# Optimization experiments

Hardware: AMD Instinct MI355X
Metric: run time of the kernel (lower is better)

## Reference

```python
import math
import jax, jax.numpy as jnp
import numpy as np

GRAIN = 300   # bilinear / grain dim (gpconv output channels)
PAD = 4       # explicit zero padding before each conv1d / conv2d
POOL = 40     # adaptive pool target (mf_model_pool_dim)

def conv1d_k2(x, w, b):
    # x: [B, L, Cin], w: [Cout, Cin, 2] -> [B, L-1, Cout]
    return (jnp.einsum('blc,oc->blo', x[:, :-1], w[:, :, 0])
            + jnp.einsum('blc,oc->blo', x[:, 1:], w[:, :, 1]) + b)

def kmax_last(x, k):
    # torch-style k-max pooling: top-k values along last axis, original order kept
    idx = jnp.sort(jax.lax.top_k(x, k)[1], axis=-1)
    return jnp.take_along_axis(x, idx, axis=-1)

def kmax_len(x, k):
    # k-max pooling over the length axis (axis=1) of [B, L, C]
    return jnp.swapaxes(kmax_last(jnp.swapaxes(x, 1, 2), k), 1, 2)

def adaptive_max_1d(x, out, axis):
    # torch AdaptiveMaxPool semantics along one axis; windows precomputed statically
    L = x.shape[axis]
    r = np.arange(out)
    starts = (r * L) // out
    ends = -((-(r + 1) * L) // out)
    maxw = int((ends - starts).max())
    off = starts[:, None] + np.arange(maxw)[None, :]
    mask = jnp.asarray(off < ends[:, None])
    idxs = np.minimum(off, L - 1)
    xm = jnp.moveaxis(x, axis, -1)
    g = jnp.where(mask, xm[..., idxs], -jnp.inf)
    return jnp.moveaxis(g.max(-1), -1, axis)

def conv2d_p4(x, w, b):
    y = jax.lax.conv_general_dilated(x, w, (1, 1), [(PAD, PAD), (PAD, PAD)],
                                     dimension_numbers=('NCHW', 'OIHW', 'NCHW'))
    return y + b[None, :, None, None]

def gp_tower(x, w1, b1, w2, b2, w3, b3, k1, k2):
    # multigranular conv tower: zero-pad(4) -> conv1d(k=2) -> tanh -> k-max pool
    g0 = kmax_last(x, GRAIN)                      # [B, L, 300]
    def block(z, w, b, k):
        z = jnp.pad(z, ((0, 0), (PAD, PAD), (0, 0)))
        return kmax_len(jnp.tanh(conv1d_k2(z, w, b)), k)
    p1 = block(x, w1, b1, k1)                     # [B, k1, 300]
    p2 = block(p1, w2, b2, k2)                    # [B, k2, 300]
    p3 = block(p2, w3, b3, 1)                     # [B, 1, 300]
    return jnp.concatenate([g0, p1, p2, p3], axis=1)

def _forward(query, pos_doc, neg_docs, qw1, qb1, qw2, qb2, qw3, qb3,
             dw1, db1, dw2, db2, dw3, db3, bw, bb,
             mw1, mb1, mw2, mb2, mw3, mb3, lw, lb):
    B, Lq, _ = query.shape
    S, _, Ld, _ = neg_docs.shape
    kq1, kq2 = max(4, math.ceil(2 * Lq / 3)), max(4, math.ceil(Lq / 3))
    kd1, kd2 = max(4, math.ceil(2 * Ld / 3)), max(4, math.ceil(Ld / 3))
    qg = gp_tower(query, qw1, qb1, qw2, qb2, qw3, qb3, kq1, kq2)   # [B, Nq, 300]
    docs = jnp.concatenate([pos_doc[None], neg_docs], 0).reshape((S + 1) * B, Ld, -1)
    dg = gp_tower(docs, dw1, db1, dw2, db2, dw3, db3, kd1, kd2)    # [(S+1)B, Nd, 300]
    Nq, Nd = qg.shape[1], dg.shape[1]
    dg = dg.reshape(S + 1, B, Nd, GRAIN)
    # batched bilinear matching + sigmoid (replaces the O(Nq*Nd) per-pair loop)
    qt = jnp.einsum('bqd,de->bqe', qg, bw)
    M = jax.nn.sigmoid(jnp.einsum('bqe,sbje->sbqj', qt, dg) + bb[0])
    M = M.reshape((S + 1) * B, Nq, Nd)
    x = adaptive_max_1d(adaptive_max_1d(M, POOL, 1), POOL, 2)[:, None]  # [N,1,40,40]
    for w, b in ((mw1, mb1), (mw2, mb2), (mw3, mb3)):
        x = jax.nn.sigmoid(conv2d_p4(x, w, b))
        x = adaptive_max_1d(adaptive_max_1d(x, POOL, 2), POOL, 3)
        x = x.max(axis=1, keepdims=True)          # k-max(k=1) over channels
    feat = x[:, 0]                                # [N, 40, 40]
    h = jax.nn.sigmoid(jnp.einsum('nij,j->ni', feat, lw[0]) + lb[0])
    s = jax.nn.sigmoid(h @ lw[0] + lb[0])
    return s.reshape(S + 1, B)                    # row 0 = pos-doc scores

def setup_inputs():
    ks = jax.random.split(jax.random.key(0), 26)
    def n(i, shape, s=0.05):
        return jax.random.normal(ks[i], shape, dtype=jnp.float32) * s
    return dict(
        query=jax.random.normal(ks[0], (16, 239, 1024), dtype=jnp.float32),
        pos_doc=jax.random.normal(ks[1], (16, 479, 1024), dtype=jnp.float32),
        neg_docs=jax.random.normal(ks[2], (4, 16, 479, 1024), dtype=jnp.float32),
        qw1=n(3, (300, 1024, 2)), qb1=n(4, (300,)),
        qw2=n(5, (300, 300, 2)), qb2=n(6, (300,)),
        qw3=n(7, (300, 300, 2)), qb3=n(8, (300,)),
        dw1=n(9, (300, 1024, 2)), db1=n(10, (300,)),
        dw2=n(11, (300, 300, 2)), db2=n(12, (300,)),
        dw3=n(13, (300, 300, 2)), db3=n(14, (300,)),
        bw=n(15, (300, 300)), bb=n(16, (1,)),
        mw1=n(17, (50, 1, 2, 2)), mb1=n(18, (50,)),
        mw2=n(19, (50, 1, 2, 2)), mb2=n(20, (50,)),
        mw3=n(21, (50, 1, 2, 2)), mb3=n(22, (50,)),
        lw=n(23, (1, 40)), lb=n(24, (1,)),
    )

def reference(query, pos_doc, neg_docs, qw1, qb1, qw2, qb2, qw3, qb3,
              dw1, db1, dw2, db2, dw3, db3, bw, bb,
              mw1, mb1, mw2, mb2, mw3, mb3, lw, lb):
    return _forward(query, pos_doc, neg_docs, qw1, qb1, qw2, qb2, qw3, qb3,
                    dw1, db1, dw2, db2, dw3, db3, bw, bb,
                    mw1, mb1, mw2, mb2, mw3, mb3, lw, lb)
```

## Files before the change

### kernel.cpp

```cpp
#include <hip/hip_runtime.h>
#include <hip/hip_bf16.h>
#include <math.h>

typedef unsigned long long ull;
typedef unsigned int uint;
typedef unsigned short ushort_t;

typedef short bf16x8 __attribute__((ext_vector_type(8)));
typedef float floatx4 __attribute__((ext_vector_type(4)));

__device__ inline ushort_t f2b(float f) {
    uint u = __float_as_uint(f);
    u = u + 0x7fffu + ((u >> 16) & 1u);
    return (ushort_t)(u >> 16);
}

__device__ inline uint kmap16(ushort_t u) {
    return (u & 0x8000u) ? (uint)((~u) & 0xFFFFu) : (uint)(u | 0x8000u);
}
__device__ inline ushort_t kinv16(uint k) {
    return (k & 0x8000u) ? (ushort_t)(k ^ 0x8000u) : (ushort_t)((~k) & 0xFFFFu);
}

__device__ inline void async_copy16(const void* g, void* l) {
    __builtin_amdgcn_global_load_lds(
        (const __attribute__((address_space(1))) void*)g,
        (__attribute__((address_space(3))) void*)l, 16, 0, 0);
}

__global__ void prep_w2_kernel(const float* __restrict__ w, ushort_t* __restrict__ Wb,
                               int C, int CPAD) {
    int total = 320 * 2 * CPAD;
    for (int i = blockIdx.x * blockDim.x + threadIdx.x; i < total;
         i += gridDim.x * blockDim.x) {
        int n = i / (2 * CPAD);
        int rem = i - n * 2 * CPAD;
        int t = rem / CPAD, c = rem - t * CPAD;
        float v = (n < 300 && c < C) ? w[((size_t)n * C + c) * 2 + t] : 0.f;
        Wb[i] = f2b(v);
    }
}

__global__ void prep_bw_kernel(const float* __restrict__ bw, ushort_t* __restrict__ bwb) {
    int i = blockIdx.x * 256 + threadIdx.x;
    if (i >= 320 * 320) return;
    int e = i / 320, d = i - e * 320;
    bwb[i] = (e < 300 && d < 300) ? f2b(bw[d * 300 + e]) : (ushort_t)0;
}

__global__ __launch_bounds__(256) void x_pad_bf16_kernel(
    const float* __restrict__ src, const float* __restrict__ src2, int split_n,
    long long s_nstr, int Lin, ushort_t* __restrict__ dst, int rows)
{
    int r = blockIdx.x, n = blockIdx.y;
    const float* sp = (split_n > 0 && n >= split_n)
                          ? src2 + (size_t)(n - split_n) * s_nstr
                          : src + (size_t)n * s_nstr;
    int g = r - 4;
    ushort_t* dp = dst + ((size_t)n * rows + r) * 1024;
    int c = threadIdx.x * 4;
    ushort4 o = {0, 0, 0, 0};
    if (g >= 0 && g < Lin) {
        float4 v = *(const float4*)&sp[(size_t)g * 1024 + c];
        o.x = f2b(v.x); o.y = f2b(v.y); o.z = f2b(v.z); o.w = f2b(v.w);
    }
    *(ushort4*)&dp[c] = o;
}

template <int CP>
__global__ __launch_bounds__(256, 2) void conv_lds_kernel(
    const ushort_t* __restrict__ xq, long long xq_nstr,
    const ushort_t* __restrict__ xd, long long xd_nstr,
    const ushort_t* __restrict__ Wq, const ushort_t* __restrict__ Wd,
    const float* __restrict__ bq, const float* __restrict__ bd,
    int Lout_q, int Lout_d, int mtiles_q,
    ushort_t* __restrict__ yt)
{
    constexpr int CH = CP / 32;
    constexpr int K2 = 2 * CP;
    __shared__ ushort_t Abuf[2][65 * 32];

    int mt = blockIdx.x, n = blockIdx.y;
    bool isq = (n < 16);
    if (isq && mt >= mtiles_q) return;
    const ushort_t* x = isq ? xq + (size_t)n * xq_nstr
                            : xd + (size_t)(n - 16) * xd_nstr;
    const ushort_t* W = isq ? Wq : Wd;
    const float* bias = isq ? bq : bd;
    int Lout = isq ? Lout_q : Lout_d;
    int l0 = mt * 64;

    int tid = threadIdx.x, wid = tid >> 6, lane = tid & 63;
    int wn = wid * 80;
    int lrow = lane & 15, quad = lane >> 4;

    const ushort_t* g0 = x + (size_t)(l0 + (tid >> 2)) * CP + (tid & 3) * 8;
    const ushort_t* g1 = x + (size_t)(l0 + 64) * CP + (tid & 3) * 8;

    const ushort_t* Bb = W + (size_t)(wn + lrow) * K2 + quad * 8;

    floatx4 acc[4][5];
#pragma unroll
    for (int i = 0; i < 4; i++)
#pragma unroll
        for (int j = 0; j < 5; j++) acc[i][j] = (floatx4){0.f, 0.f, 0.f, 0.f};

    {
        char* lb = (char*)&Abuf[0][0];
        async_copy16(g0, lb + wid * 1024);
        if (tid < 4) async_copy16(g1, lb + 4096);
    }

    for (int c = 0; c < CH; c++) {
        __syncthreads();
        int c0 = c * 32;

        bf16x8 bfr[2][5];
#pragma unroll
        for (int t = 0; t < 2; t++)
#pragma unroll
            for (int ns = 0; ns < 5; ns++)
                bfr[t][ns] = *(const bf16x8*)&Bb[(size_t)(ns * 16) * K2 + t * CP + c0];

        if (c + 1 < CH) {
            char* lb = (char*)&Abuf[(c + 1) & 1][0];
            async_copy16(g0 + c0 + 32, lb + wid * 1024);
            if (tid < 4) async_copy16(g1 + c0 + 32, lb + 4096);
        }

        const char* ab = (const char*)&Abuf[c & 1][0];
        bf16x8 af[2][4];
#pragma unroll
        for (int t = 0; t < 2; t++)
#pragma unroll
            for (int ms = 0; ms < 4; ms++)
                af[t][ms] = *(const bf16x8*)(ab + (ms * 16 + lrow + t) * 64 + quad * 16);

#pragma unroll
        for (int t = 0; t < 2; t++)
#pragma unroll
            for (int ms = 0; ms < 4; ms++)
#pragma unroll
                for (int ns = 0; ns < 5; ns++)
                    acc[ms][ns] = __builtin_amdgcn_mfma_f32_16x16x32_bf16(
                        af[t][ms], bfr[t][ns], acc[ms][ns], 0, 0, 0);
    }

    ushort_t* yp = yt + (size_t)n * 488 * 320;
#pragma unroll
    for (int ns = 0; ns < 5; ns++) {
        int o = wn + ns * 16 + lrow;
        if (o >= 300) continue;
        float bo = bias[o];
#pragma unroll
        for (int ms = 0; ms < 4; ms++)
#pragma unroll
            for (int r = 0; r < 4; r++) {
                int l = l0 + ms * 16 + quad * 4 + r;
                if (l < Lout)
                    yp[(size_t)l * 320 + o] = f2b(tanhf(acc[ms][ns][r] + bo));
            }
    }
}

template <int EPT>
__global__ __launch_bounds__(256) void topk16_kernel(
    const ushort_t* __restrict__ src, int CC,
    long long s_n, long long s_c, long long s_e,
    int L, int k,
    ushort_t* __restrict__ out1, long long o1_off, long long o1_n,
    long long o1_c, long long o1_e,
    ushort_t* __restrict__ out2, long long o2_off, long long o2_n,
    long long o2_c, long long o2_e)
{
    __shared__ uint sbuf[257];
    __shared__ uint wtot[4];
    __shared__ uint bsel[2];
    __shared__ uint wsum[4];

    int row = blockIdx.x;
    int n = row / CC, c = row - n * CC;
    const ushort_t* sp = src + (size_t)n * s_n + (size_t)c * s_c;

    int tid = threadIdx.x, lane = tid & 63, wid = tid >> 6;
    int base = tid * EPT;

    uint key[EPT];
    if (EPT == 4 && s_e == 1) {
        ushort4 v = *(const ushort4*)&sp[base];
        key[0] = kmap16(v.x); key[1] = kmap16(v.y);
        key[2] = kmap16(v.z); key[3] = kmap16(v.w);
    } else {
#pragma unroll
        for (int e = 0; e < EPT; e++) {
            int i = base + e;
            key[e] = (i < L) ? kmap16(sp[(size_t)i * s_e]) : 0u;
        }
    }

    uint pmask = 0, pval = 0, rem = (uint)k;
#pragma unroll
    for (int shift = 8; shift >= 0; shift -= 8) {
        sbuf[tid] = 0;
        __syncthreads();
#pragma unroll
        for (int e = 0; e < EPT; e++) {
            int i = base + e;
            if (i < L && (key[e] & pmask) == pval)
                atomicAdd(&sbuf[(key[e] >> shift) & 255], 1u);
        }
        __syncthreads();
        uint sfx = sbuf[tid];
#pragma unroll
        for (int off = 1; off < 64; off <<= 1) {
            uint u2 = __shfl_down(sfx, off);
            if (lane + off < 64) sfx += u2;
        }
        if (lane == 0) wtot[wid] = sfx;
        __syncthreads();
        uint hi = 0;
        for (int w = wid + 1; w < 4; w++) hi += wtot[w];
        sbuf[tid] = sfx + hi;
        if (tid == 0) sbuf[256] = 0;
        __syncthreads();
        uint cg = sbuf[tid], cgn = sbuf[tid + 1];
        if (cg >= rem && cgn < rem) { bsel[0] = (uint)tid; bsel[1] = rem - cgn; }
        __syncthreads();
        pval |= bsel[0] << shift;
        pmask |= 0xFFu << shift;
        rem = bsel[1];
        __syncthreads();
    }

    const uint T = pval;
    uint gtc = 0, eqc = 0;
#pragma unroll
    for (int e = 0; e < EPT; e++) {
        int i = base + e;
        if (i < L) {
            gtc += (key[e] > T) ? 1u : 0u;
            eqc += (key[e] == T) ? 1u : 0u;
        }
    }
    uint pack = (gtc << 16) | eqc;
    uint incl = pack;
#pragma unroll
    for (int off = 1; off < 64; off <<= 1) {
        uint u2 = __shfl_up(incl, off);
        if (lane >= off) incl += u2;
    }
    uint excl = incl - pack;
    if (lane == 63) wsum[wid] = incl;
    __syncthreads();
    uint badd = 0;
    for (int w = 0; w < wid; w++) badd += wsum[w];
    excl += badd;
    uint gt_before = excl >> 16, eq_before = excl & 0xffffu;

    ushort_t* dp1 = out1 + (size_t)o1_off + (size_t)n * o1_n + (size_t)c * o1_c;
    ushort_t* dp2 = out2 ? out2 + (size_t)o2_off + (size_t)n * o2_n + (size_t)c * o2_c
                         : (ushort_t*)0;
#pragma unroll
    for (int e = 0; e < EPT; e++) {
        int i = base + e;
        if (i >= L) break;
        uint kk = key[e];
        if (kk > T) {
            uint pos = gt_before + (eq_before < rem ? eq_before : rem);
            ushort_t v = kinv16(kk);
            dp1[(size_t)pos * o1_e] = v;
            if (dp2) dp2[(size_t)pos * o2_e] = v;
            gt_before++;
        } else if (kk == T) {
            if (eq_before < rem) {
                uint pos = gt_before + eq_before;
                ushort_t v = kinv16(kk);
                dp1[(size_t)pos * o1_e] = v;
                if (dp2) dp2[(size_t)pos * o2_e] = v;
            }
            eq_before++;
        }
    }
}

__global__ __launch_bounds__(256) void qt_mfma_kernel(
    const ushort_t* __restrict__ qgb, const ushort_t* __restrict__ bwb,
    ushort_t* __restrict__ qtb)
{
    int mt = blockIdx.x, b = blockIdx.y;
    int tid = threadIdx.x, wid = tid >> 6, lane = tid & 63;
    int wn = wid * 80, lrow = lane & 15, quad = lane >> 4;

    const ushort_t* A = qgb + ((size_t)b * 480 + mt * 48 + lrow) * 320 + quad * 8;
    const ushort_t* B = bwb + (size_t)(wn + lrow) * 320 + quad * 8;

    floatx4 acc[3][5];
#pragma unroll
    for (int i = 0; i < 3; i++)
#pragma unroll
        for (int j = 0; j < 5; j++) acc[i][j] = (floatx4){0.f, 0.f, 0.f, 0.f};

#pragma unroll 5
    for (int c0 = 0; c0 < 320; c0 += 32) {
        bf16x8 af[3], bfr[5];
#pragma unroll
        for (int ms = 0; ms < 3; ms++)
            af[ms] = *(const bf16x8*)&A[(size_t)(ms * 16) * 320 + c0];
#pragma unroll
        for (int ns = 0; ns < 5; ns++)
            bfr[ns] = *(const bf16x8*)&B[(size_t)(ns * 16) * 320 + c0];
#pragma unroll
        for (int ms = 0; ms < 3; ms++)
#pragma unroll
            for (int ns = 0; ns < 5; ns++)
                acc[ms][ns] = __builtin_amdgcn_mfma_f32_16x16x32_bf16(
                    af[ms], bfr[ns], acc[ms][ns], 0, 0, 0);
    }

    ushort_t* out = qtb + ((size_t)b * 480 + mt * 48) * 320;
#pragma unroll
    for (int ms = 0; ms < 3; ms++)
#pragma unroll
        for (int ns = 0; ns < 5; ns++)
#pragma unroll
            for (int r = 0; r < 4; r++)
                out[(size_t)(ms * 16 + quad * 4 + r) * 320 + wn + ns * 16 + lrow] =
                    f2b(acc[ms][ns][r]);
}

__global__ __launch_bounds__(256) void mpool_mfma_kernel(
    const ushort_t* __restrict__ qtb16, const ushort_t* __restrict__ dgb16,
    const float* __restrict__ bb, float* __restrict__ mp)
{
    __shared__ float pool[2 * 12 * 192];

    int jb = blockIdx.x;
    int qb = blockIdx.y;
    int n  = blockIdx.z;
    int b  = n & 15;

    int tid = threadIdx.x;
    int wid = tid >> 6, lane = tid & 63;
    int wm2 = wid >> 1;
    int wm = wm2 * 48, wn = (wid & 1) * 96;
    int lrow = lane & 15, quad = lane >> 4;

    const ushort_t* Abase = qtb16 + ((size_t)b * 480 + qb * 96 + wm) * 320 + quad * 8;
    const ushort_t* Bbase = dgb16 + ((size_t)n * 960 + jb * 192 + wn) * 320 + quad * 8;

    floatx4 acc[3][6];
#pragma unroll
    for (int i = 0; i < 3; i++)
#pragma unroll
        for (int j = 0; j < 6; j++) acc[i][j] = (floatx4){0.f, 0.f, 0.f, 0.f};

#pragma unroll 2
    for (int c0 = 0; c0 < 320; c0 += 32) {
        bf16x8 af[3], bfr[6];
#pragma unroll
        for (int mt = 0; mt < 3; mt++)
            af[mt] = *(const bf16x8*)&Abase[(size_t)(mt * 16 + lrow) * 320 + c0];
#pragma unroll
        for (int nt = 0; nt < 6; nt++)
            bfr[nt] = *(const bf16x8*)&Bbase[(size_t)(nt * 16 + lrow) * 320 + c0];
#pragma unroll
        for (int mt = 0; mt < 3; mt++)
#pragma unroll
            for (int nt = 0; nt < 6; nt++)
                acc[mt][nt] = __builtin_amdgcn_mfma_f32_16x16x32_bf16(
                    af[mt], bfr[nt], acc[mt][nt], 0, 0, 0);
    }

#pragma unroll
    for (int mt = 0; mt < 3; mt++) {
        int g = mt * 4 + quad;
#pragma unroll
        for (int nt = 0; nt < 6; nt++) {
            floatx4 a = acc[mt][nt];
            float rm = fmaxf(fmaxf(a[0], a[1]), fmaxf(a[2], a[3]));
            pool[(wm2 * 12 + g) * 192 + wn + nt * 16 + lrow] = rm;
        }
    }
    __syncthreads();

    if (tid < 64) {
        int qw = tid >> 3, jw = tid & 7;
        int slab = qw >> 2, w = qw & 3;
        float m = -INFINITY;
        const float* pp = &pool[(slab * 12 + w * 3) * 192 + jw * 24];
        for (int g = 0; g < 3; g++)
            for (int cc = 0; cc < 24; cc++)
                m = fmaxf(m, pp[g * 192 + cc]);
        float sig = 1.f / (1.f + expf(-(m + bb[0])));
        mp[(size_t)n * 1600 + (size_t)(qb * 8 + qw) * 40 + (jb * 8 + jw)] = sig;
    }
}

#define OCG 10
__global__ __launch_bounds__(256) void convblock_atomic_kernel(
    const float* __restrict__ X, const float* __restrict__ w,
    const float* __restrict__ bias, uint* __restrict__ Y)
{
    __shared__ float xp[48 * 48];
    __shared__ float ys[47 * 47];
    __shared__ float t1[40 * 47];
    __shared__ float outacc[1600];

    int n = blockIdx.x, t = threadIdx.x;
    int oc0 = blockIdx.y * OCG;
    const float* xn = X + (size_t)n * 1600;
    for (int i = t; i < 48 * 48; i += 256) {
        int r = i / 48, c = i - r * 48;
        int rr = r - 4, cc = c - 4;
        xp[i] = (rr >= 0 && rr < 40 && cc >= 0 && cc < 40) ? xn[rr * 40 + cc] : 0.f;
    }
    for (int i = t; i < 1600; i += 256) outacc[i] = 0.f;
    __syncthreads();

    for (int oc = oc0; oc < oc0 + OCG; oc++) {
        float w00 = w[oc * 4 + 0], w01 = w[oc * 4 + 1];
        float w10 = w[oc * 4 + 2], w11 = w[oc * 4 + 3];
        float bo = bias[oc];
        for (int i = t; i < 47 * 47; i += 256) {
            int r = i / 47, c = i - r * 47;
            float v = xp[r * 48 + c] * w00 + xp[r * 48 + c + 1] * w01
                    + xp[(r + 1) * 48 + c] * w10 + xp[(r + 1) * 48 + c + 1] * w11 + bo;
            ys[i] = 1.f / (1.f + expf(-v));
        }
        __syncthreads();
        for (int i = t; i < 40 * 47; i += 256) {
            int r = i / 47, c = i - r * 47;
            int s = (47 * r) / 40, e = (47 * (r + 1) + 39) / 40;
            float m = ys[s * 47 + c];
            for (int x = s + 1; x < e; x++) m = fmaxf(m, ys[x * 47 + c]);
            t1[i] = m;
        }
        __syncthreads();
        for (int i = t; i < 1600; i += 256) {
            int r = i / 40, c = i - r * 40;
            int s = (47 * c) / 40, e = (47 * (c + 1) + 39) / 40;
            float m = t1[r * 47 + s];
            for (int x = s + 1; x < e; x++) m = fmaxf(m, t1[r * 47 + x]);
            outacc[i] = fmaxf(outacc[i], m);
        }
        __syncthreads();
    }
    for (int i = t; i < 1600; i += 256)
        atomicMax(&Y[(size_t)n * 1600 + i], __float_as_uint(outacc[i]));
}

__global__ __launch_bounds__(64) void head_kernel(
    const float* __restrict__ feat, const float* __restrict__ lw,
    const float* __restrict__ lb, float* __restrict__ out)
{
    __shared__ float hs[40];
    int n = blockIdx.x, t = threadIdx.x;
    const float* f = feat + (size_t)n * 1600;
    if (t < 40) {
        float a = 0.f;
        for (int j = 0; j < 40; j++) a += f[t * 40 + j] * lw[j];
        hs[t] = 1.f / (1.f + expf(-(a + lb[0])));
    }
    __syncthreads();
    if (t == 0) {
        float a = 0.f;
        for (int i = 0; i < 40; i++) a += hs[i] * lw[i];
        out[n] = 1.f / (1.f + expf(-(a + lb[0])));
    }
}

extern "C" void kernel_launch(void* const* d_in, const int* in_sizes, int n_in,
                              void* d_out, int out_size, void* d_ws, size_t ws_size,
                              hipStream_t stream) {
    const float* query    = (const float*)d_in[0];
    const float* pos_doc  = (const float*)d_in[1];
    const float* neg_docs = (const float*)d_in[2];
    const float* qw1 = (const float*)d_in[3];  const float* qb1 = (const float*)d_in[4];
    const float* qw2 = (const float*)d_in[5];  const float* qb2 = (const float*)d_in[6];
    const float* qw3 = (const float*)d_in[7];  const float* qb3 = (const float*)d_in[8];
    const float* dw1 = (const float*)d_in[9];  const float* db1 = (const float*)d_in[10];
    const float* dw2 = (const float*)d_in[11]; const float* db2 = (const float*)d_in[12];
    const float* dw3 = (const float*)d_in[13]; const float* db3 = (const float*)d_in[14];
    const float* bw  = (const float*)d_in[15]; const float* bb  = (const float*)d_in[16];
    const float* mw1 = (const float*)d_in[17]; const float* mb1 = (const float*)d_in[18];
    const float* mw2 = (const float*)d_in[19]; const float* mb2 = (const float*)d_in[20];
    const float* mw3 = (const float*)d_in[21]; const float* mb3 = (const float*)d_in[22];
    const float* lw  = (const float*)d_in[23]; const float* lb  = (const float*)d_in[24];

    float* ws = (float*)d_ws;
    ushort_t* qw1b  = (ushort_t*)(ws + 0);
    ushort_t* qw2b  = (ushort_t*)(ws + 327680);
    ushort_t* qw3b  = (ushort_t*)(ws + 430080);
    ushort_t* dw1b  = (ushort_t*)(ws + 532480);
    ushort_t* dw2b  = (ushort_t*)(ws + 860160);
    ushort_t* dw3b  = (ushort_t*)(ws + 962560);
    ushort_t* bwb   = (ushort_t*)(ws + 1064960);
    ushort_t* qgb16 = (ushort_t*)(ws + 1116160);
    ushort_t* dgb16 = (ushort_t*)(ws + 2344960);
    ushort_t* yt    = (ushort_t*)(ws + 14632960);
    ushort_t* qxb   = (ushort_t*)(ws + 22128640);
    ushort_t* p1q   = (ushort_t*)(ws + 22128640);
    ushort_t* p2q   = (ushort_t*)(ws + 22640640);
    ushort_t* dxb   = (ushort_t*)(ws + 24291328);
    ushort_t* p1d   = (ushort_t*)(ws + 24291328);
    ushort_t* p2d   = (ushort_t*)(ws + 28899328);
    ushort_t* qtb16 = (ushort_t*)(ws + 31459328);
    float*    mp    = ws + 32688128;
    float*    ya    = ws + 32816128;
    float*    yb    = ws + 32944128;
    float*    yc    = ws + 33072128;

    prep_w2_kernel<<<1280, 256, 0, stream>>>(qw1, qw1b, 1024, 1024);
    prep_w2_kernel<<<400, 256, 0, stream>>>(qw2, qw2b, 300, 320);
    prep_w2_kernel<<<400, 256, 0, stream>>>(qw3, qw3b, 300, 320);
    prep_w2_kernel<<<1280, 256, 0, stream>>>(dw1, dw1b, 1024, 1024);
    prep_w2_kernel<<<400, 256, 0, stream>>>(dw2, dw2b, 300, 320);
    prep_w2_kernel<<<400, 256, 0, stream>>>(dw3, dw3b, 300, 320);
    prep_bw_kernel<<<400, 256, 0, stream>>>(bw, bwb);

    {
        dim3 g(264, 16);
        x_pad_bf16_kernel<<<g, 256, 0, stream>>>(query, nullptr, 0,
                                                 239LL * 1024, 239, qxb, 264);
    }
    {
        dim3 g(520, 80);
        x_pad_bf16_kernel<<<g, 256, 0, stream>>>(pos_doc, neg_docs, 16,
                                                 479LL * 1024, 479, dxb, 520);
    }

    topk16_kernel<4><<<16 * 239, 256, 0, stream>>>(
        qxb + 4 * 1024, 239, 264LL * 1024, 1024, 1, 1024, 300,
        qgb16, 0, 480LL * 320, 320, 1,
        nullptr, 0, 0, 0, 0);
    topk16_kernel<4><<<80 * 479, 256, 0, stream>>>(
        dxb + 4 * 1024, 479, 520LL * 1024, 1024, 1, 1024, 300,
        dgb16, 0, 960LL * 320, 320, 1,
        nullptr, 0, 0, 0, 0);

    {
        dim3 g(8, 96);
        conv_lds_kernel<1024><<<g, 256, 0, stream>>>(
            qxb, 264LL * 1024, dxb, 520LL * 1024,
            qw1b, dw1b, qb1, db1, 246, 486, 4, yt);
    }

    hipMemsetAsync(p1q, 0, 16 * 200 * 320 * 2, stream);
    hipMemsetAsync(p2q, 0, 16 * 104 * 320 * 2, stream);
    hipMemsetAsync(p1d, 0, (size_t)80 * 360 * 320 * 2, stream);
    hipMemsetAsync(p2d, 0, (size_t)80 * 200 * 320 * 2, stream);
    hipMemsetAsync(ya, 0, 80 * 1600 * 4, stream);
    hipMemsetAsync(yb, 0, 80 * 1600 * 4, stream);
    hipMemsetAsync(yc, 0, 80 * 1600 * 4, stream);

    topk16_kernel<1><<<16 * 300, 256, 0, stream>>>(
        yt, 300, 488LL * 320, 1, 320, 246, 160,
        qgb16, 239LL * 320, 480LL * 320, 1, 320,
        p1q, 4LL * 320, 200LL * 320, 1, 320);
    topk16_kernel<2><<<80 * 300, 256, 0, stream>>>(
        yt + (size_t)16 * 488 * 320, 300, 488LL * 320, 1, 320, 486, 320,
        dgb16, 479LL * 320, 960LL * 320, 1, 320,
        p1d, 4LL * 320, 360LL * 320, 1, 320);

    {
        dim3 g(6, 96);
        conv_lds_kernel<320><<<g, 256, 0, stream>>>(
            p1q, 200LL * 320, p1d, 360LL * 320,
            qw2b, dw2b, qb2, db2, 167, 327, 3, yt);
    }

    topk16_kernel<1><<<16 * 300, 256, 0, stream>>>(
        yt, 300, 488LL * 320, 1, 320, 167, 80,
        qgb16, 399LL * 320, 480LL * 320, 1, 320,
        p2q, 4LL * 320, 104LL * 320, 1, 320);
    topk16_kernel<2><<<80 * 300, 256, 0, stream>>>(
        yt + (size_t)16 * 488 * 320, 300, 488LL * 320, 1, 320, 327, 160,
        dgb16, 799LL * 320, 960LL * 320, 1, 320,
        p2d, 4LL * 320, 200LL * 320, 1, 320);

    {
        dim3 g(3, 96);
        conv_lds_kernel<320><<<g, 256, 0, stream>>>(
            p2q, 104LL * 320, p2d, 200LL * 320,
            qw3b, dw3b, qb3, db3, 87, 167, 2, yt);
    }

    topk16_kernel<1><<<16 * 300, 256, 0, stream>>>(
        yt, 300, 488LL * 320, 1, 320, 87, 1,
        qgb16, 479LL * 320, 480LL * 320, 1, 320,
        nullptr, 0, 0, 0, 0);
    topk16_kernel<1><<<80 * 300, 256, 0, stream>>>(
        yt + (size_t)16 * 488 * 320, 300, 488LL * 320, 1, 320, 167, 1,
        dgb16, 959LL * 320, 960LL * 320, 1, 320,
        nullptr, 0, 0, 0, 0);

    {
        dim3 g(10, 16);
        qt_mfma_kernel<<<g, 256, 0, stream>>>(qgb16, bwb, qtb16);
    }
    {
        dim3 g(5, 5, 80);
        mpool_mfma_kernel<<<g, 256, 0, stream>>>(qtb16, dgb16, bb, mp);
    }

    {
        dim3 g(80, 5);
        convblock_atomic_kernel<<<g, 256, 0, stream>>>(mp, mw1, mb1, (uint*)ya);
        convblock_atomic_kernel<<<g, 256, 0, stream>>>(ya, mw2, mb2, (uint*)yb);
        convblock_atomic_kernel<<<g, 256, 0, stream>>>(yb, mw3, mb3, (uint*)yc);
    }
    head_kernel<<<80, 64, 0, stream>>>(yc, lw, lb, (float*)d_out);
}
```

Measured before the change: 1.313 ms.

## Triple-buffer conv LDS pipeline with swizzled A tiles and fragment-ordered weights

Reworks the conv GEMM main loop into a three-slot LDS ring with a two-deep async prefetch and register double-buffered B fragments. It uses explicit vmcnt waits plus raw barriers instead of __syncthreads, and raises wave priority around the MFMA block. The A tile gets an XOR swizzle to avoid LDS bank conflicts. Weights are pre-permuted into MFMA fragment order so each lane issues contiguous 16-byte loads. The hand-tuned waitcnt and sched_barrier masks add correctness risk if the outstanding-load count is wrong, and the loop assumes CH is even.

```diff
diff --git a/kernel.cpp b/kernel.cpp
--- a/kernel.cpp
+++ b/kernel.cpp
@@ -29,14 +29,20 @@
 }
 
 __global__ void prep_w2_kernel(const float* __restrict__ w, ushort_t* __restrict__ Wb,
-                               int C, int CPAD) {
-    int total = 320 * 2 * CPAD;
+                               int C, int CP) {
+    int CHn = CP / 32;
+    int total = CHn * 2 * 20 * 512;
     for (int i = blockIdx.x * blockDim.x + threadIdx.x; i < total;
          i += gridDim.x * blockDim.x) {
-        int n = i / (2 * CPAD);
-        int rem = i - n * 2 * CPAD;
-        int t = rem / CPAD, c = rem - t * CPAD;
-        float v = (n < 300 && c < C) ? w[((size_t)n * C + c) * 2 + t] : 0.f;
+        int e = i & 7;
+        int lane = (i >> 3) & 63;
+        int rest = i >> 9;
+        int g = rest % 20;
+        int tc = rest / 20;
+        int t = tc & 1, c = tc >> 1;
+        int o = g * 16 + (lane & 15);
+        int ch = c * 32 + (lane >> 4) * 8 + e;
+        float v = (o < 300 && ch < C) ? w[((size_t)o * C + ch) * 2 + t] : 0.f;
         Wb[i] = f2b(v);
     }
 }
@@ -77,8 +83,8 @@
     ushort_t* __restrict__ yt)
 {
     constexpr int CH = CP / 32;
-    constexpr int K2 = 2 * CP;
-    __shared__ ushort_t Abuf[2][65 * 32];
+    constexpr int BUFB = 65 * 64;
+    __shared__ ushort_t Abuf[3][65 * 32];
 
     int mt = blockIdx.x, n = blockIdx.y;
     bool isq = (n < 16);
@@ -94,10 +100,21 @@
     int wn = wid * 80;
     int lrow = lane & 15, quad = lane >> 4;
 
-    const ushort_t* g0 = x + (size_t)(l0 + (tid >> 2)) * CP + (tid & 3) * 8;
-    const ushort_t* g1 = x + (size_t)(l0 + 64) * CP + (tid & 3) * 8;
-
-    const ushort_t* Bb = W + (size_t)(wn + lrow) * K2 + quad * 8;
+    int srow = tid >> 2;
+    int sslot = (tid & 3) ^ ((tid >> 3) & 3);
+    const ushort_t* gMain = x + (size_t)(l0 + srow) * CP + sslot * 8;
+    const ushort_t* gXtra = x + (size_t)(l0 + 64) * CP + wid * 8;
+
+    const ushort_t* Bw = W + ((size_t)wid * 5) * 512 + lane * 8;
+
+    int offA[2][4];
+#pragma unroll
+    for (int t = 0; t < 2; t++)
+#pragma unroll
+        for (int ms = 0; ms < 4; ms++) {
+            int r = ms * 16 + lrow + t;
+            offA[t][ms] = r * 64 + ((quad ^ ((r >> 1) & 3)) << 4);
+        }
 
     floatx4 acc[4][5];
 #pragma unroll
@@ -105,45 +122,70 @@
 #pragma unroll
         for (int j = 0; j < 5; j++) acc[i][j] = (floatx4){0.f, 0.f, 0.f, 0.f};
 
-    {
-        char* lb = (char*)&Abuf[0][0];
-        async_copy16(g0, lb + wid * 1024);
-        if (tid < 4) async_copy16(g1, lb + 4096);
-    }
-
-    for (int c = 0; c < CH; c++) {
-        __syncthreads();
-        int c0 = c * 32;
-
-        bf16x8 bfr[2][5];
+    char* lds0 = (char*)&Abuf[0][0];
+
+    auto STAGE = [&](int cc, int slot) {
+        char* lb = lds0 + slot * BUFB;
+        async_copy16(gMain + cc * 32, lb + wid * 1024);
+        if (lane == 0) async_copy16(gXtra + cc * 32, lb + 4096 + wid * 16);
+    };
+    auto LOADB = [&](bf16x8 (&bf)[2][5], int cc) {
 #pragma unroll
         for (int t = 0; t < 2; t++)
 #pragma unroll
             for (int ns = 0; ns < 5; ns++)
-                bfr[t][ns] = *(const bf16x8*)&Bb[(size_t)(ns * 16) * K2 + t * CP + c0];
-
-        if (c + 1 < CH) {
-            char* lb = (char*)&Abuf[(c + 1) & 1][0];
-            async_copy16(g0 + c0 + 32, lb + wid * 1024);
-            if (tid < 4) async_copy16(g1 + c0 + 32, lb + 4096);
-        }
-
-        const char* ab = (const char*)&Abuf[c & 1][0];
-        bf16x8 af[2][4];
-#pragma unroll
-        for (int t = 0; t < 2; t++)
+                bf[t][ns] = *(const bf16x8*)(Bw + (size_t)((cc * 2 + t) * 20 + ns) * 512);
+    };
+    auto COMPUTE = [&](bf16x8 (&bf)[2][5], int rslot) {
+        const char* ab = lds0 + rslot * BUFB;
+        __builtin_amdgcn_s_setprio(1);
+#pragma unroll
+        for (int t = 0; t < 2; t++) {
+            bf16x8 af[4];
 #pragma unroll
             for (int ms = 0; ms < 4; ms++)
-                af[t][ms] = *(const bf16x8*)(ab + (ms * 16 + lrow + t) * 64 + quad * 16);
-
-#pragma unroll
-        for (int t = 0; t < 2; t++)
+                af[ms] = *(const bf16x8*)(ab + offA[t][ms]);
 #pragma unroll
             for (int ms = 0; ms < 4; ms++)
 #pragma unroll
                 for (int ns = 0; ns < 5; ns++)
                     acc[ms][ns] = __builtin_amdgcn_mfma_f32_16x16x32_bf16(
-                        af[t][ms], bfr[t][ns], acc[ms][ns], 0, 0, 0);
+                        af[ms], bf[t][ns], acc[ms][ns], 0, 0, 0);
+        }
+        __builtin_amdgcn_s_setprio(0);
+    };
+    auto WAITBAR = [&]() {
+        asm volatile("s_waitcnt vmcnt(10)" ::: "memory");
+        __builtin_amdgcn_s_barrier();
+        __builtin_amdgcn_sched_barrier(0);
+    };
+
+    bf16x8 bA[2][5], bB[2][5];
+
+    STAGE(0, 0);
+    LOADB(bA, 0);
+    STAGE(1, 1);
+
+    int sl = 0;
+    for (int c = 0; c < CH; c += 2) {
+        int rA = sl;
+        int rB = rA + 1; if (rB == 3) rB = 0;
+        int wA = rB + 1; if (wA == 3) wA = 0;
+        int wB = rA;
+
+        WAITBAR();
+        LOADB(bB, c + 1);
+        __builtin_amdgcn_sched_barrier(0x38F);
+        if (c + 2 < CH) STAGE(c + 2, wA);
+        COMPUTE(bA, rA);
+
+        WAITBAR();
+        if (c + 2 < CH) LOADB(bA, c + 2);
+        __builtin_amdgcn_sched_barrier(0x38F);
+        if (c + 3 < CH) STAGE(c + 3, wB);
+        COMPUTE(bB, rB);
+
+        sl = wA;
     }
 
     ushort_t* yp = yt + (size_t)n * 488 * 320;
```

New measurement: 1.244 ms. -5.3%, faster.
